# Optimization experiments

Measured on AMD Instinct MI355X. Metric: run time of the kernel, lower is better.

Reference implementation:

```python
import jax, jax.numpy as jnp
import numpy as np

NUM_SEQS = 4
Q_LEN = 512          # new query tokens per sequence (chunked prefill)
SEQ_LEN = 2048       # total tokens per sequence (context + query)
NUM_Q_HEADS = 32
NUM_KV_HEADS = 8
HEAD_SIZE = 128
BLOCK_SIZE = 32
BLOCKS_PER_SEQ = SEQ_LEN // BLOCK_SIZE          # 64
NUM_BLOCKS = NUM_SEQS * BLOCKS_PER_SEQ          # 256 physical blocks


def setup_inputs() -> dict:
    key = jax.random.key(0)
    k1, k2, k3 = jax.random.split(key, 3)
    query = jax.random.normal(k1, (NUM_SEQS * Q_LEN, NUM_Q_HEADS, HEAD_SIZE), dtype=jnp.float32)
    key_cache = jax.random.normal(k2, (NUM_BLOCKS, BLOCK_SIZE, NUM_KV_HEADS, HEAD_SIZE), dtype=jnp.float32)
    value_cache = jax.random.normal(k3, (NUM_BLOCKS, BLOCK_SIZE, NUM_KV_HEADS, HEAD_SIZE), dtype=jnp.float32)
    # each sequence owns a contiguous run of physical blocks (any permutation works)
    block_tables = jnp.arange(NUM_BLOCKS, dtype=jnp.int32).reshape(NUM_SEQS, BLOCKS_PER_SEQ)
    seq_lens = jnp.full((NUM_SEQS,), SEQ_LEN, dtype=jnp.int32)
    query_start_loc = jnp.arange(NUM_SEQS + 1, dtype=jnp.int32) * Q_LEN
    return {"query": query, "key_cache": key_cache, "value_cache": value_cache,
            "block_tables": block_tables, "seq_lens": seq_lens,
            "query_start_loc": query_start_loc}


def reference(query, key_cache, value_cache, block_tables, seq_lens, query_start_loc):
    # paged/unified attention, base config: causal, GQA, no window/alibi/softcap/sinks/quant
    B, NB = block_tables.shape
    BS = key_cache.shape[1]
    total_q, Hq, D = query.shape
    Kvh = key_cache.shape[2]
    G = Hq // Kvh                       # num_queries_per_kv
    Lq = total_q // B                   # uniform query len per seq (matches query_start_loc)
    S = NB * BS                         # max kv length covered by block table
    scale = D ** -0.5

    q = query.reshape(B, Lq, Kvh, G, D)
    # gather paged KV: [B, NB, BS, Kvh, D] -> [B, S, Kvh, D]
    k = key_cache[block_tables].reshape(B, S, Kvh, D)
    v = value_cache[block_tables].reshape(B, S, Kvh, D)

    scores = jnp.einsum('blkgd,bskd->blkgs', q, k) * scale  # [B, Lq, Kvh, G, S]

    # absolute query positions: context_len + local pos, context_len = seq_len - Lq
    q_abs = (seq_lens - Lq)[:, None] + jnp.arange(Lq, dtype=seq_lens.dtype)[None, :]  # [B, Lq]
    kpos = jnp.arange(S, dtype=seq_lens.dtype)
    causal = kpos[None, None, :] <= q_abs[:, :, None]                 # key <= query pos
    valid = kpos[None, None, :] < seq_lens[:, None, None]             # key within seq
    mask = causal & valid                                             # [B, Lq, S]

    neg_inf = jnp.asarray(-jnp.inf, scores.dtype)
    scores = jnp.where(mask[:, :, None, None, :], scores, neg_inf)
    p = jax.nn.softmax(scores, axis=-1)
    out = jnp.einsum('blkgs,bskd->blkgd', p, v)                       # [B, Lq, Kvh, G, D]
    return out.reshape(total_q, Hq, D)
```

## Files before the change

### kernel.cpp

```cpp
#include <hip/hip_runtime.h>
#include <hip/hip_bf16.h>

typedef __bf16 bf16;
typedef __attribute__((ext_vector_type(8))) __bf16 bf16x8;
typedef __attribute__((ext_vector_type(4))) __bf16 bf16x4;
typedef __attribute__((ext_vector_type(4))) float f32x4;

static constexpr int NSEQ = 4;
static constexpr int LQ   = 512;
static constexpr int HQN  = 32;
static constexpr int HKVN = 8;
static constexpr int GQ   = 4;
static constexpr int DH   = 128;
static constexpr int BPS  = 64;
static constexpr int SKV  = 2048;
static constexpr int KVB  = 64;
static constexpr int QBL  = 32;

__device__ __forceinline__ bf16x8 cvt8(const float4& a, const float4& b) {
  bf16x8 o;
  o[0] = (bf16)a.x; o[1] = (bf16)a.y; o[2] = (bf16)a.z; o[3] = (bf16)a.w;
  o[4] = (bf16)b.x; o[5] = (bf16)b.y; o[6] = (bf16)b.z; o[7] = (bf16)b.w;
  return o;
}

__global__ void prep_k(const float* __restrict__ kc, const int* __restrict__ bt,
                       bf16* __restrict__ kb) {
  int e = (blockIdx.x * 256 + threadIdx.x) * 8;
  int d = e & 127;
  int s = (e >> 7) & 2047;
  int h = (e >> 18) & 7;
  int b = e >> 21;
  int pb = bt[b * BPS + (s >> 5)];
  const float* src = kc + (((size_t)pb * 32 + (s & 31)) * 8 + h) * 128 + d;
  float4 a = *(const float4*)src;
  float4 c = *(const float4*)(src + 4);
  *(bf16x8*)(kb + e) = cvt8(a, c);
}

__global__ void prep_vt(const float* __restrict__ vc, const int* __restrict__ bt,
                        bf16* __restrict__ vt) {
  __shared__ __align__(16) bf16 T[64][136];
  int bid = blockIdx.x;
  int st = bid & 31;
  int h  = (bid >> 5) & 7;
  int b  = bid >> 8;
  int tid = threadIdx.x;
  {
    int s  = tid >> 2;
    int d0 = (tid & 3) * 32;
    int sg = st * 64 + s;
    int pb = bt[b * BPS + (sg >> 5)];
    const float* src = vc + (((size_t)pb * 32 + (sg & 31)) * 8 + h) * 128 + d0;
#pragma unroll
    for (int k = 0; k < 4; ++k) {
      float4 a = *(const float4*)(src + 8 * k);
      float4 c = *(const float4*)(src + 8 * k + 4);
      *(bf16x8*)&T[s][d0 + 8 * k] = cvt8(a, c);
    }
  }
  __syncthreads();
  {
    int d  = tid & 127;
    int g2 = tid >> 7;
    bf16* dst = vt + (((size_t)(b * 8 + h)) * 128 + d) * SKV + st * 64 + g2 * 32;
#pragma unroll
    for (int k = 0; k < 4; ++k) {
      bf16x8 o;
#pragma unroll
      for (int j = 0; j < 8; ++j) o[j] = T[g2 * 32 + k * 8 + j][d];
      *(bf16x8*)(dst + 8 * k) = o;
    }
  }
}

template <bool WS>
__global__ __launch_bounds__(256, 2)
void attn_kern(const float* __restrict__ q, const float* __restrict__ kc,
               const float* __restrict__ vc, const int* __restrict__ bt,
               const int* __restrict__ seq_lens, const bf16* __restrict__ kb,
               const bf16* __restrict__ vtb, float* __restrict__ out) {
  __shared__ __align__(16) bf16 Kl[64][136];
  __shared__ __align__(16) bf16 Vl[128][72];
  __shared__ __align__(16) bf16 Pl[4][32][72];

  int bid = (int)blockIdx.x;
  bid = (bid & 7) * 64 + (bid >> 3);
  int qt = bid & 15;
  int h  = (bid >> 4) & 7;
  int b  = bid >> 7;
  int lb = qt * QBL;

  int tid  = (int)threadIdx.x;
  int w    = tid >> 6;
  int lane = tid & 63;
  int lq   = lane & 15;
  int lg   = lane >> 4;

  int ctx = seq_lens[b] - LQ;
  int nt  = (ctx + lb + QBL + KVB - 1) / KVB;

  const float CEXP = 0.08838834764831843f * 1.44269504088896340f;

  int hq = h * GQ + w;
  bf16x8 qf[2][4];
#pragma unroll
  for (int n = 0; n < 2; ++n) {
    const float* qp = q + (((size_t)(b * LQ + lb + n * 16 + lq)) * HQN + hq) * DH + lg * 8;
#pragma unroll
    for (int kk = 0; kk < 4; ++kk) {
      float4 a = *(const float4*)(qp + kk * 32);
      float4 c = *(const float4*)(qp + kk * 32 + 4);
      qf[n][kk] = cvt8(a, c);
    }
  }

  f32x4 accO[2][8];
  f32x4 zero = {0.f, 0.f, 0.f, 0.f};
#pragma unroll
  for (int m = 0; m < 2; ++m)
#pragma unroll
    for (int nd = 0; nd < 8; ++nd) accO[m][nd] = zero;
  float mrun[2] = {-1e30f, -1e30f};
  float lrun[2] = {0.f, 0.f};

  const int* btr = bt + b * BPS;

  for (int t = 0; t < nt; ++t) {
    if (WS) {
      const bf16* ks = kb + (((size_t)(b * 8 + h)) * SKV + t * 64) * DH;
      int s  = tid >> 2;
      int d0 = (tid & 3) * 32;
#pragma unroll
      for (int k = 0; k < 4; ++k)
        *(bf16x8*)&Kl[s][d0 + 8 * k] = *(const bf16x8*)(ks + s * DH + d0 + 8 * k);
      const bf16* vs = vtb + (((size_t)(b * 8 + h)) * DH) * SKV + t * 64;
      int d   = tid >> 1;
      int sg2 = (tid & 1) * 32;
#pragma unroll
      for (int k = 0; k < 4; ++k)
        *(bf16x8*)&Vl[d][sg2 + 8 * k] = *(const bf16x8*)(vs + (size_t)d * SKV + sg2 + 8 * k);
    } else {
      int s  = tid >> 2;
      int d0 = (tid & 3) * 32;
      int pb = btr[t * 2 + (s >> 5)];
      const float* ksrc = kc + (((size_t)pb * 32 + (s & 31)) * 8 + h) * 128 + d0;
#pragma unroll
      for (int k = 0; k < 4; ++k) {
        float4 a = *(const float4*)(ksrc + 8 * k);
        float4 c = *(const float4*)(ksrc + 8 * k + 4);
        *(bf16x8*)&Kl[s][d0 + 8 * k] = cvt8(a, c);
      }
      int d  = tid & 127;
      int sh = tid >> 7;
      int pbv = btr[t * 2 + sh];
      const float* vsrc = vc + (((size_t)pbv * 32) * 8 + h) * 128 + d;
#pragma unroll
      for (int k = 0; k < 8; ++k) {
        bf16x4 o;
#pragma unroll
        for (int j = 0; j < 4; ++j) o[j] = (bf16)vsrc[(size_t)(k * 4 + j) * 1024];
        *(bf16x4*)&Vl[d][sh * 32 + 4 * k] = o;
      }
    }
    __syncthreads();

    f32x4 accS[4][2];
#pragma unroll
    for (int m = 0; m < 4; ++m)
#pragma unroll
      for (int n = 0; n < 2; ++n) accS[m][n] = zero;
#pragma unroll
    for (int m = 0; m < 4; ++m) {
      bf16x8 ak[4];
#pragma unroll
      for (int kk = 0; kk < 4; ++kk)
        ak[kk] = *(const bf16x8*)&Kl[m * 16 + lq][kk * 32 + lg * 8];
#pragma unroll
      for (int n = 0; n < 2; ++n)
#pragma unroll
        for (int kk = 0; kk < 4; ++kk)
          accS[m][n] = __builtin_amdgcn_mfma_f32_16x16x32_bf16(ak[kk], qf[n][kk], accS[m][n], 0, 0, 0);
    }

    if (t * KVB + KVB - 1 > ctx + lb) {
#pragma unroll
      for (int m = 0; m < 4; ++m) {
        int sg = t * 64 + m * 16 + lg * 4;
#pragma unroll
        for (int n = 0; n < 2; ++n) {
          int qpos = ctx + lb + n * 16 + lq;
#pragma unroll
          for (int r = 0; r < 4; ++r)
            if (sg + r > qpos) accS[m][n][r] = -1e30f;
        }
      }
    }

#pragma unroll
    for (int n = 0; n < 2; ++n) {
      float mx = accS[0][n][0];
#pragma unroll
      for (int m = 0; m < 4; ++m)
#pragma unroll
        for (int r = 0; r < 4; ++r) mx = fmaxf(mx, accS[m][n][r]);
      mx = fmaxf(mx, __shfl_xor(mx, 16));
      mx = fmaxf(mx, __shfl_xor(mx, 32));
      float mnew = fmaxf(mrun[n], mx);
      float corr = exp2f((mrun[n] - mnew) * CEXP);
      mrun[n] = mnew;
      float psum = 0.f;
#pragma unroll
      for (int m = 0; m < 4; ++m) {
        bf16x4 pk;
#pragma unroll
        for (int r = 0; r < 4; ++r) {
          float p = exp2f((accS[m][n][r] - mnew) * CEXP);
          psum += p;
          pk[r] = (bf16)p;
        }
        *(bf16x4*)&Pl[w][n * 16 + lq][m * 16 + lg * 4] = pk;
      }
      lrun[n] = lrun[n] * corr + psum;
      float cb[4];
#pragma unroll
      for (int r = 0; r < 4; ++r) cb[r] = __shfl(corr, lg * 4 + r);
#pragma unroll
      for (int nd = 0; nd < 8; ++nd)
#pragma unroll
        for (int r = 0; r < 4; ++r) accO[n][nd][r] *= cb[r];
    }

    asm volatile("s_waitcnt lgkmcnt(0)" ::: "memory");

    bf16x8 ap[2][2];
#pragma unroll
    for (int m2 = 0; m2 < 2; ++m2)
#pragma unroll
      for (int ks = 0; ks < 2; ++ks)
        ap[m2][ks] = *(const bf16x8*)&Pl[w][m2 * 16 + lq][ks * 32 + lg * 8];
#pragma unroll
    for (int nd = 0; nd < 8; ++nd) {
      bf16x8 bv0 = *(const bf16x8*)&Vl[nd * 16 + lq][lg * 8];
      bf16x8 bv1 = *(const bf16x8*)&Vl[nd * 16 + lq][32 + lg * 8];
#pragma unroll
      for (int m2 = 0; m2 < 2; ++m2) {
        accO[m2][nd] = __builtin_amdgcn_mfma_f32_16x16x32_bf16(ap[m2][0], bv0, accO[m2][nd], 0, 0, 0);
        accO[m2][nd] = __builtin_amdgcn_mfma_f32_16x16x32_bf16(ap[m2][1], bv1, accO[m2][nd], 0, 0, 0);
      }
    }
    __syncthreads();
  }

#pragma unroll
  for (int n = 0; n < 2; ++n) {
    lrun[n] += __shfl_xor(lrun[n], 16);
    lrun[n] += __shfl_xor(lrun[n], 32);
    lrun[n] = 1.f / lrun[n];
  }
#pragma unroll
  for (int m2 = 0; m2 < 2; ++m2) {
    float rb[4];
#pragma unroll
    for (int r = 0; r < 4; ++r) rb[r] = __shfl(lrun[m2], lg * 4 + r);
#pragma unroll
    for (int r = 0; r < 4; ++r) {
      float* op = out + (((size_t)(b * LQ + lb + m2 * 16 + lg * 4 + r)) * HQN + hq) * DH + lq;
#pragma unroll
      for (int nd = 0; nd < 8; ++nd) op[nd * 16] = accO[m2][nd][r] * rb[r];
    }
  }
}

extern "C" void kernel_launch(void* const* d_in, const int* in_sizes, int n_in,
                              void* d_out, int out_size, void* d_ws, size_t ws_size,
                              hipStream_t stream) {
  const float* q  = (const float*)d_in[0];
  const float* kc = (const float*)d_in[1];
  const float* vc = (const float*)d_in[2];
  const int* bt   = (const int*)d_in[3];
  const int* sl   = (const int*)d_in[4];
  float* out = (float*)d_out;

  size_t half = (size_t)NSEQ * HKVN * SKV * DH;
  size_t need = 2 * half * sizeof(bf16);
  if (ws_size >= need) {
    bf16* kb = (bf16*)d_ws;
    bf16* vt = kb + half;
    hipLaunchKernelGGL(prep_k, dim3(4096), dim3(256), 0, stream, kc, bt, kb);
    hipLaunchKernelGGL(prep_vt, dim3(1024), dim3(256), 0, stream, vc, bt, vt);
    hipLaunchKernelGGL((attn_kern<true>), dim3(512), dim3(256), 0, stream,
                       q, kc, vc, bt, sl, kb, vt, out);
  } else {
    hipLaunchKernelGGL((attn_kern<false>), dim3(512), dim3(256), 0, stream,
                       q, kc, vc, bt, sl, (const bf16*)nullptr, (const bf16*)nullptr, out);
  }
}
```

Measured before the change: 137.1 us.

## Prefetch KV tiles into registers, skip softmax rescale, rebalance causal block mapping

The bf16 workspace path now loads the next K/V tile into registers while the current tile is computed, then stores it to shared memory between barriers. This hides global-load latency. The online softmax skips the max update and accumulator rescale when no wave-wide max grows past a threshold, a lazy rescaling that keeps exponents bounded. Block indexing is remapped so paired workgroups take query tiles i and 15-i, spreading causal work evenly across XCDs. The risks are higher register pressure from the prefetch buffers and an extra barrier per iteration.

```diff
diff --git a/kernel.cpp b/kernel.cpp
--- a/kernel.cpp
+++ b/kernel.cpp
@@ -85,11 +85,16 @@
   __shared__ __align__(16) bf16 Pl[4][32][72];
 
   int bid = (int)blockIdx.x;
-  bid = (bid & 7) * 64 + (bid >> 3);
-  int qt = bid & 15;
-  int h  = (bid >> 4) & 7;
-  int b  = bid >> 7;
-  int lb = qt * QBL;
+  int hi  = bid >> 8;
+  int u   = bid & 255;
+  int xcd = u & 7;
+  int k2  = u >> 3;
+  int c   = (k2 >> 3) | (xcd << 2);
+  int i   = k2 & 7;
+  int qt  = hi ? (15 - i) : i;
+  int h   = c & 7;
+  int b   = c >> 3;
+  int lb  = qt * QBL;
 
   int tid  = (int)threadIdx.x;
   int w    = tid >> 6;
@@ -101,6 +106,7 @@
   int nt  = (ctx + lb + QBL + KVB - 1) / KVB;
 
   const float CEXP = 0.08838834764831843f * 1.44269504088896340f;
+  const float TH8  = 8.0f / CEXP;
 
   int hq = h * GQ + w;
   bf16x8 qf[2][4];
@@ -110,8 +116,8 @@
 #pragma unroll
     for (int kk = 0; kk < 4; ++kk) {
       float4 a = *(const float4*)(qp + kk * 32);
-      float4 c = *(const float4*)(qp + kk * 32 + 4);
-      qf[n][kk] = cvt8(a, c);
+      float4 c2 = *(const float4*)(qp + kk * 32 + 4);
+      qf[n][kk] = cvt8(a, c2);
     }
   }
 
@@ -125,46 +131,29 @@
   float lrun[2] = {0.f, 0.f};
 
   const int* btr = bt + b * BPS;
-
-  for (int t = 0; t < nt; ++t) {
-    if (WS) {
-      const bf16* ks = kb + (((size_t)(b * 8 + h)) * SKV + t * 64) * DH;
-      int s  = tid >> 2;
-      int d0 = (tid & 3) * 32;
-#pragma unroll
-      for (int k = 0; k < 4; ++k)
-        *(bf16x8*)&Kl[s][d0 + 8 * k] = *(const bf16x8*)(ks + s * DH + d0 + 8 * k);
-      const bf16* vs = vtb + (((size_t)(b * 8 + h)) * DH) * SKV + t * 64;
-      int d   = tid >> 1;
-      int sg2 = (tid & 1) * 32;
-#pragma unroll
-      for (int k = 0; k < 4; ++k)
-        *(bf16x8*)&Vl[d][sg2 + 8 * k] = *(const bf16x8*)(vs + (size_t)d * SKV + sg2 + 8 * k);
-    } else {
-      int s  = tid >> 2;
-      int d0 = (tid & 3) * 32;
-      int pb = btr[t * 2 + (s >> 5)];
-      const float* ksrc = kc + (((size_t)pb * 32 + (s & 31)) * 8 + h) * 128 + d0;
-#pragma unroll
-      for (int k = 0; k < 4; ++k) {
-        float4 a = *(const float4*)(ksrc + 8 * k);
-        float4 c = *(const float4*)(ksrc + 8 * k + 4);
-        *(bf16x8*)&Kl[s][d0 + 8 * k] = cvt8(a, c);
-      }
-      int d  = tid & 127;
-      int sh = tid >> 7;
-      int pbv = btr[t * 2 + sh];
-      const float* vsrc = vc + (((size_t)pbv * 32) * 8 + h) * 128 + d;
-#pragma unroll
-      for (int k = 0; k < 8; ++k) {
-        bf16x4 o;
-#pragma unroll
-        for (int j = 0; j < 4; ++j) o[j] = (bf16)vsrc[(size_t)(k * 4 + j) * 1024];
-        *(bf16x4*)&Vl[d][sh * 32 + 4 * k] = o;
-      }
-    }
-    __syncthreads();
-
+  const bf16* kbase = WS ? kb  + (size_t)(b * 8 + h) * SKV * DH : nullptr;
+  const bf16* vbase = WS ? vtb + (size_t)(b * 8 + h) * DH * SKV : nullptr;
+
+  int ks_ = tid >> 2, kd0 = (tid & 3) * 32;
+  int vd_ = tid >> 1, vs0 = (tid & 1) * 32;
+
+  bf16x8 kpre[4], vpre[4];
+  auto ldKV = [&](int t) {
+    const bf16* ks = kbase + ((size_t)t * 64 + ks_) * DH + kd0;
+#pragma unroll
+    for (int k = 0; k < 4; ++k) kpre[k] = *(const bf16x8*)(ks + 8 * k);
+    const bf16* vs = vbase + (size_t)vd_ * SKV + t * 64 + vs0;
+#pragma unroll
+    for (int k = 0; k < 4; ++k) vpre[k] = *(const bf16x8*)(vs + 8 * k);
+  };
+  auto stKV = [&]() {
+#pragma unroll
+    for (int k = 0; k < 4; ++k) *(bf16x8*)&Kl[ks_][kd0 + 8 * k] = kpre[k];
+#pragma unroll
+    for (int k = 0; k < 4; ++k) *(bf16x8*)&Vl[vd_][vs0 + 8 * k] = vpre[k];
+  };
+
+  auto compute = [&](int t) {
     f32x4 accS[4][2];
 #pragma unroll
     for (int m = 0; m < 4; ++m)
@@ -206,29 +195,32 @@
         for (int r = 0; r < 4; ++r) mx = fmaxf(mx, accS[m][n][r]);
       mx = fmaxf(mx, __shfl_xor(mx, 16));
       mx = fmaxf(mx, __shfl_xor(mx, 32));
-      float mnew = fmaxf(mrun[n], mx);
-      float corr = exp2f((mrun[n] - mnew) * CEXP);
-      mrun[n] = mnew;
+      if (!__all(mx <= mrun[n] + TH8)) {
+        float mnew = fmaxf(mrun[n], mx);
+        float corr = exp2f((mrun[n] - mnew) * CEXP);
+        mrun[n] = mnew;
+        lrun[n] *= corr;
+        float cb[4];
+#pragma unroll
+        for (int r = 0; r < 4; ++r) cb[r] = __shfl(corr, lg * 4 + r);
+#pragma unroll
+        for (int nd = 0; nd < 8; ++nd)
+#pragma unroll
+          for (int r = 0; r < 4; ++r) accO[n][nd][r] *= cb[r];
+      }
       float psum = 0.f;
 #pragma unroll
       for (int m = 0; m < 4; ++m) {
         bf16x4 pk;
 #pragma unroll
         for (int r = 0; r < 4; ++r) {
-          float p = exp2f((accS[m][n][r] - mnew) * CEXP);
+          float p = exp2f((accS[m][n][r] - mrun[n]) * CEXP);
           psum += p;
           pk[r] = (bf16)p;
         }
         *(bf16x4*)&Pl[w][n * 16 + lq][m * 16 + lg * 4] = pk;
       }
-      lrun[n] = lrun[n] * corr + psum;
-      float cb[4];
-#pragma unroll
-      for (int r = 0; r < 4; ++r) cb[r] = __shfl(corr, lg * 4 + r);
-#pragma unroll
-      for (int nd = 0; nd < 8; ++nd)
-#pragma unroll
-        for (int r = 0; r < 4; ++r) accO[n][nd][r] *= cb[r];
+      lrun[n] += psum;
     }
 
     asm volatile("s_waitcnt lgkmcnt(0)" ::: "memory");
@@ -237,8 +229,8 @@
 #pragma unroll
     for (int m2 = 0; m2 < 2; ++m2)
 #pragma unroll
-      for (int ks = 0; ks < 2; ++ks)
-        ap[m2][ks] = *(const bf16x8*)&Pl[w][m2 * 16 + lq][ks * 32 + lg * 8];
+      for (int ks3 = 0; ks3 < 2; ++ks3)
+        ap[m2][ks3] = *(const bf16x8*)&Pl[w][m2 * 16 + lq][ks3 * 32 + lg * 8];
 #pragma unroll
     for (int nd = 0; nd < 8; ++nd) {
       bf16x8 bv0 = *(const bf16x8*)&Vl[nd * 16 + lq][lg * 8];
@@ -249,7 +241,51 @@
         accO[m2][nd] = __builtin_amdgcn_mfma_f32_16x16x32_bf16(ap[m2][1], bv1, accO[m2][nd], 0, 0, 0);
       }
     }
+  };
+
+  if (WS) {
+    ldKV(0);
+    stKV();
     __syncthreads();
+    for (int t = 0; t < nt; ++t) {
+      bool more = (t + 1 < nt);
+      if (more) ldKV(t + 1);
+      compute(t);
+      if (more) {
+        __syncthreads();
+        stKV();
+        __syncthreads();
+      }
+    }
+  } else {
+    for (int t = 0; t < nt; ++t) {
+      {
+        int s  = tid >> 2;
+        int d0 = (tid & 3) * 32;
+        int pb = btr[t * 2 + (s >> 5)];
+        const float* ksrc = kc + (((size_t)pb * 32 + (s & 31)) * 8 + h) * 128 + d0;
+#pragma unroll
+        for (int k = 0; k < 4; ++k) {
+          float4 a = *(const float4*)(ksrc + 8 * k);
+          float4 c2 = *(const float4*)(ksrc + 8 * k + 4);
+          *(bf16x8*)&Kl[s][d0 + 8 * k] = cvt8(a, c2);
+        }
+        int d  = tid & 127;
+        int sh = tid >> 7;
+        int pbv = btr[t * 2 + sh];
+        const float* vsrc = vc + (((size_t)pbv * 32) * 8 + h) * 128 + d;
+#pragma unroll
+        for (int k = 0; k < 8; ++k) {
+          bf16x4 o;
+#pragma unroll
+          for (int j = 0; j < 4; ++j) o[j] = (bf16)vsrc[(size_t)(k * 4 + j) * 1024];
+          *(bf16x4*)&Vl[d][sh * 32 + 4 * k] = o;
+        }
+      }
+      __syncthreads();
+      compute(t);
+      __syncthreads();
+    }
   }
 
 #pragma unroll
```

Result: faster. 123.6 us (-9.8%).
